# Kernel tuning notes

Hardware: AMD Instinct MI355X
Metric: run time of the kernel (lower is better)

## Reference

```python
import jax, jax.numpy as jnp
import numpy as np

D_CONV = 4
D_STATE = 32
DT_RANK = 16


def setup_inputs() -> dict:
    key = jax.random.key(0)
    ks = jax.random.split(key, 12)
    B, D, L, DI = 4, 256, 1024, 256
    s = 0.02
    return {
        "x": jax.random.normal(ks[0], (B, D, L), jnp.float32),
        "Win": jax.random.normal(ks[1], (4, D, 2 * DI), jnp.float32) * s,
        "Wconv": jax.random.normal(ks[2], (4, DI, D_CONV), jnp.float32) * 0.2,
        "bconv": jnp.zeros((4, DI), jnp.float32),
        "Wxp": jax.random.normal(ks[3], (4, DI, DT_RANK + 2 * D_STATE), jnp.float32) * s,
        "Wdt": jax.random.normal(ks[4], (4, DT_RANK, DI), jnp.float32) * s,
        "bdt": jnp.full((4, DI), -2.0, jnp.float32),
        "Alog": jnp.tile(jnp.log(jnp.arange(1, D_STATE + 1, dtype=jnp.float32))[None, None, :], (4, DI, 1)),
        "Dskip": jnp.ones((4, DI), jnp.float32),
        "Wout": jax.random.normal(ks[5], (4, DI, D), jnp.float32) * s,
        "Wg": jax.random.normal(ks[6], (2, L, L), jnp.float32) * 0.01,
        "bg": jnp.zeros((2, L), jnp.float32),
        "alpha": jnp.ones((2,), jnp.float32),
        "gamma": jnp.ones((2, L), jnp.float32),
        "beta": jnp.zeros((2, L), jnp.float32),
    }


def _selective_scan(u, dt, Bm, Cm, A):
    # u, dt: [B,L,di]; Bm, Cm: [B,L,N]; A: [di,N]
    dBu = dt * u
    def step(h, inp):
        dt_t, dbu_t, B_t, C_t = inp  # [B,di],[B,di],[B,N],[B,N]
        h = jnp.exp(dt_t[:, :, None] * A) * h + dbu_t[:, :, None] * B_t[:, None, :]
        y = jnp.einsum('bdn,bn->bd', h, C_t)
        return h, y
    xs = (jnp.moveaxis(dt, 1, 0), jnp.moveaxis(dBu, 1, 0),
          jnp.moveaxis(Bm, 1, 0), jnp.moveaxis(Cm, 1, 0))
    h0 = jnp.zeros((u.shape[0], A.shape[0], A.shape[1]), u.dtype)
    _, ys = jax.lax.scan(step, h0, xs)  # ys: [L,B,di]
    return jnp.moveaxis(ys, 0, 1)


def _mamba_layer(x_bdl, Win, Wconv, bconv, Wxp, Wdt, bdt, Alog, Dskip, Wout):
    x = jnp.swapaxes(x_bdl, 1, 2)  # [B,L,D]
    L = x.shape[1]
    u, z = jnp.split(x @ Win, 2, axis=-1)  # each [B,L,di]
    up = jnp.pad(u, ((0, 0), (D_CONV - 1, 0), (0, 0)))
    u = sum(up[:, k:k + L, :] * Wconv[:, k] for k in range(D_CONV)) + bconv
    u = jax.nn.silu(u)
    proj = u @ Wxp
    dtp = proj[..., :DT_RANK]
    Bm = proj[..., DT_RANK:DT_RANK + D_STATE]
    Cm = proj[..., DT_RANK + D_STATE:]
    dt = jax.nn.softplus(dtp @ Wdt + bdt)
    y = _selective_scan(u, dt, Bm, Cm, -jnp.exp(Alog)) + u * Dskip
    y = y * jax.nn.silu(z)
    return jnp.swapaxes(y @ Wout, 1, 2)  # [B,d_out,L]


def _forward(x, Win, Wconv, bconv, Wxp, Wdt, bdt, Alog, Dskip, Wout, Wg, bg, alpha, gamma, beta):
    def branch(inp, i0, i1, j):
        h = _mamba_layer(inp, Win[i0], Wconv[i0], bconv[i0], Wxp[i0], Wdt[i0], bdt[i0], Alog[i0], Dskip[i0], Wout[i0])
        h = _mamba_layer(h, Win[i1], Wconv[i1], bconv[i1], Wxp[i1], Wdt[i1], bdt[i1], Alog[i1], Dskip[i1], Wout[i1])
        return gamma[j] * jnp.tanh(alpha[j] * h) + beta[j]  # DyTanh over last dim
    def gate(j):
        return jax.nn.sigmoid(jnp.einsum('bdl,ml->bdm', x, Wg[j]) + bg[j])
    m = branch(x, 0, 1, 0) * gate(0)
    rx = jnp.flip(x, axis=-1)
    rm = branch(rx, 2, 3, 1) * gate(1)
    return m + jnp.flip(rm, axis=-1)


def reference(x, Win, Wconv, bconv, Wxp, Wdt, bdt, Alog, Dskip, Wout, Wg, bg, alpha, gamma, beta):
    return _forward(x, Win, Wconv, bconv, Wxp, Wdt, bdt, Alog, Dskip, Wout, Wg, bg, alpha, gamma, beta)
```

## Files before the change

### kernel.cpp

```cpp
#include <hip/hip_runtime.h>


#define LSEQ 1024
#define SCAN_CL 16
#define SCAN_NC 64

#if __has_builtin(__builtin_amdgcn_exp2f)
#define EXP2(x) __builtin_amdgcn_exp2f(x)
#else
#define EXP2(x) exp2f(x)
#endif

typedef short bf16x8 __attribute__((ext_vector_type(8)));
typedef float f32x4 __attribute__((ext_vector_type(4)));

__device__ __forceinline__ float sigmoidf_(float x) { return 1.f / (1.f + __expf(-x)); }
__device__ __forceinline__ float siluf_(float x)    { return x / (1.f + __expf(-x)); }
__device__ __forceinline__ float softplusf_(float x){ return x > 20.f ? x : log1pf(__expf(x)); }

__device__ __forceinline__ unsigned short bf16rne_(float v) {
  unsigned u = __float_as_uint(v);
  return (unsigned short)((u + 0x7FFFu + ((u >> 16) & 1u)) >> 16);
}
__device__ __forceinline__ float bfto_(unsigned short h) {
  return __uint_as_float(((unsigned)h) << 16);
}
__device__ __forceinline__ void split3_(float v, unsigned short& h,
                                        unsigned short& m, unsigned short& l) {
  h = bf16rne_(v); float r = v - bfto_(h);
  m = bf16rne_(r); float r2 = r - bfto_(m);
  l = bf16rne_(r2);
}

__device__ __forceinline__ long swzi(long idx, long row) {
  return idx ^ (((row >> 1) & 3) << 3);
}

__device__ void tconv3_body(const float* __restrict__ in,
                            unsigned short* __restrict__ oh,
                            unsigned short* __restrict__ om,
                            unsigned short* __restrict__ ol,
                            int K, int N, int bx, int by, int z) {
  __shared__ float T[32][33];
  int n0 = bx * 32, k0 = by * 32;
  int tx = threadIdx.x & 31, ty = threadIdx.x >> 5;
  const float* src = in + (long)z * K * N;
#pragma unroll
  for (int m = 0; m < 4; ++m)
    T[ty + 8 * m][tx] = src[(long)(k0 + ty + 8 * m) * N + n0 + tx];
  __syncthreads();
  long obase = (long)z * N * K;
#pragma unroll
  for (int m = 0; m < 4; ++m) {
    float v = T[tx][ty + 8 * m];
    int n = n0 + ty + 8 * m;
    long o = swzi(obase + (long)n * K + k0 + tx, n);
    split3_(v, oh[o], om[o], ol[o]);
  }
}

__device__ void split3v_body(const float4* __restrict__ in,
                             unsigned short* __restrict__ oh,
                             unsigned short* __restrict__ om,
                             unsigned short* __restrict__ ol, int i) {
  float4 v = in[i];
  long b = 4L * i;
  long sb = swzi(b, b >> 10);
  ushort4 H, M, L;
  split3_(v.x, H.x, M.x, L.x); split3_(v.y, H.y, M.y, L.y);
  split3_(v.z, H.z, M.z, L.z); split3_(v.w, H.w, M.w, L.w);
  *(ushort4*)(oh + sb) = H; *(ushort4*)(om + sb) = M; *(ushort4*)(ol + sb) = L;
}

__global__ __launch_bounds__(256)
void preprocess_kernel(const float* __restrict__ x, const float* __restrict__ Wg,
                       const float* __restrict__ Win, const float* __restrict__ Wout,
                       const float* __restrict__ Alog,
                       unsigned short* __restrict__ Xh, unsigned short* __restrict__ Xm,
                       unsigned short* __restrict__ Xl,
                       unsigned short* __restrict__ XGh, unsigned short* __restrict__ XGm,
                       unsigned short* __restrict__ XGl,
                       unsigned short* __restrict__ Wgh, unsigned short* __restrict__ Wgm,
                       unsigned short* __restrict__ Wgl,
                       unsigned short* __restrict__ WinTh, unsigned short* __restrict__ WinTm,
                       unsigned short* __restrict__ WinTl,
                       unsigned short* __restrict__ WoutTh, unsigned short* __restrict__ WoutTm,
                       unsigned short* __restrict__ WoutTl,
                       float* __restrict__ Aneg) {
  const int bid = blockIdx.x;
  if (bid < 8192) {
    long idx = (long)bid * 256 + threadIdx.x;
    int d = (int)(idx & 255);
    long t = idx >> 8;
    int l = (int)(t & 1023);
    int t2 = (int)(t >> 10);
    int b = t2 & 3;
    int j = t2 >> 2;
    int lsrc = j ? (1023 - l) : l;
    float v = x[((long)(b * 256 + d)) * LSEQ + lsrc];
    long o = swzi(idx, t);
    split3_(v, Xh[o], Xm[o], Xl[o]);
  } else if (bid < 9216) {
    int i = (bid - 8192) * 256 + threadIdx.x;
    split3v_body((const float4*)x, XGh, XGm, XGl, i);
  } else if (bid < 11264) {
    int i = (bid - 9216) * 256 + threadIdx.x;
    split3v_body((const float4*)Wg, Wgh, Wgm, Wgl, i);
  } else if (bid < 11776) {
    int t = bid - 11264;
    tconv3_body(Win, WinTh, WinTm, WinTl, 256, 512, t & 15, (t >> 4) & 7, t >> 7);
  } else if (bid < 12032) {
    int t = bid - 11776;
    tconv3_body(Wout, WoutTh, WoutTm, WoutTl, 256, 256, t & 7, (t >> 3) & 7, t >> 6);
  } else {
    int idx = (bid - 12032) * 256 + threadIdx.x;
    Aneg[idx] = -__expf(Alog[idx]) * 1.4426950408889634f;
  }
}

__device__ __forceinline__ void gload16(const unsigned short* g, unsigned short* l) {
  __builtin_amdgcn_global_load_lds(
      (const __attribute__((address_space(1))) unsigned int*)g,
      (__attribute__((address_space(3))) unsigned int*)l, 16, 0, 0);
}

template <int KSPLIT>
__global__ __launch_bounds__(256)
void gemm_mfma(const unsigned short* __restrict__ Ah_g,
               const unsigned short* __restrict__ Am_g,
               const unsigned short* __restrict__ Al_g, long aZ, int lda,
               const unsigned short* __restrict__ Bh_g,
               const unsigned short* __restrict__ Bm_g,
               const unsigned short* __restrict__ Bl_g, long bZ, int ldb,
               float* __restrict__ C, long cZ, int N, int KH) {
  __shared__ unsigned short S[2][6][128 * 32];
  const int bz = blockIdx.z;
  const int z  = (KSPLIT == 2) ? (bz >> 1) : bz;
  const int kh = (KSPLIT == 2) ? (bz & 1) : 0;
  const int m0 = blockIdx.y * 128, n0 = blockIdx.x * 128;
  const int tid = threadIdx.x;

  const long khoff = (long)kh * KH;
  const long a0 = (long)z * aZ + (long)(m0 + (tid >> 2)) * lda + khoff + (tid & 3) * 8;
  const long a1 = a0 + 64L * lda;
  const long b0 = (long)z * bZ + (long)(n0 + (tid >> 2)) * ldb + khoff + (tid & 3) * 8;
  const long b1 = b0 + 64L * ldb;
  const int l0 = tid * 8, l1 = tid * 8 + 2048;

  const int lane = tid & 63, w = tid >> 6;
  const int wr = w >> 1, wc = w & 1;
  const int fr = lane & 15, g = lane >> 4;

  f32x4 acc[4][4];
#pragma unroll
  for (int i = 0; i < 4; ++i)
#pragma unroll
    for (int j = 0; j < 4; ++j)
#pragma unroll
      for (int q = 0; q < 4; ++q) acc[i][j][q] = 0.f;

#define ISSUE_TILE(B, KOFF)                                 \
  do {                                                      \
    gload16(Ah_g + a0 + (KOFF), &S[B][0][l0]);              \
    gload16(Ah_g + a1 + (KOFF), &S[B][0][l1]);              \
    gload16(Am_g + a0 + (KOFF), &S[B][1][l0]);              \
    gload16(Am_g + a1 + (KOFF), &S[B][1][l1]);              \
    gload16(Al_g + a0 + (KOFF), &S[B][2][l0]);              \
    gload16(Al_g + a1 + (KOFF), &S[B][2][l1]);              \
    gload16(Bh_g + b0 + (KOFF), &S[B][3][l0]);              \
    gload16(Bh_g + b1 + (KOFF), &S[B][3][l1]);              \
    gload16(Bm_g + b0 + (KOFF), &S[B][4][l0]);              \
    gload16(Bm_g + b1 + (KOFF), &S[B][4][l1]);              \
    gload16(Bl_g + b0 + (KOFF), &S[B][5][l0]);              \
    gload16(Bl_g + b1 + (KOFF), &S[B][5][l1]);              \
  } while (0)

  ISSUE_TILE(0, 0);
  int cur = 0;

  for (int k0 = 0; k0 < KH; k0 += 32) {
    asm volatile("s_waitcnt lgkmcnt(0)" ::: "memory");
    __builtin_amdgcn_s_barrier();
    if (k0 + 32 < KH) {
      ISSUE_TILE(cur ^ 1, k0 + 32);
      asm volatile("s_waitcnt vmcnt(12)" ::: "memory");
    } else {
      asm volatile("s_waitcnt vmcnt(0)" ::: "memory");
    }
    __builtin_amdgcn_s_barrier();
    __builtin_amdgcn_sched_barrier(0);

    bf16x8 fb[3][4];
#pragma unroll
    for (int nf = 0; nf < 4; ++nf) {
      int rb = wc * 64 + nf * 16 + fr;
      int ob = rb * 32 + ((g ^ ((rb >> 1) & 3)) << 3);
      fb[0][nf] = *(const bf16x8*)&S[cur][3][ob];
      fb[1][nf] = *(const bf16x8*)&S[cur][4][ob];
      fb[2][nf] = *(const bf16x8*)&S[cur][5][ob];
    }
#pragma unroll
    for (int mf = 0; mf < 4; ++mf) {
      int ra = wr * 64 + mf * 16 + fr;
      int oa = ra * 32 + ((g ^ ((ra >> 1) & 3)) << 3);
      bf16x8 fah = *(const bf16x8*)&S[cur][0][oa];
      bf16x8 fam = *(const bf16x8*)&S[cur][1][oa];
      bf16x8 fal = *(const bf16x8*)&S[cur][2][oa];
#pragma unroll
      for (int nf = 0; nf < 4; ++nf) {
        acc[mf][nf] = __builtin_amdgcn_mfma_f32_16x16x32_bf16(fah, fb[0][nf], acc[mf][nf], 0, 0, 0);
        acc[mf][nf] = __builtin_amdgcn_mfma_f32_16x16x32_bf16(fah, fb[1][nf], acc[mf][nf], 0, 0, 0);
        acc[mf][nf] = __builtin_amdgcn_mfma_f32_16x16x32_bf16(fam, fb[0][nf], acc[mf][nf], 0, 0, 0);
        acc[mf][nf] = __builtin_amdgcn_mfma_f32_16x16x32_bf16(fam, fb[1][nf], acc[mf][nf], 0, 0, 0);
        acc[mf][nf] = __builtin_amdgcn_mfma_f32_16x16x32_bf16(fah, fb[2][nf], acc[mf][nf], 0, 0, 0);
        acc[mf][nf] = __builtin_amdgcn_mfma_f32_16x16x32_bf16(fal, fb[0][nf], acc[mf][nf], 0, 0, 0);
      }
    }
    cur ^= 1;
  }
#undef ISSUE_TILE

  float* Cz = C + (long)bz * cZ;
#pragma unroll
  for (int mf = 0; mf < 4; ++mf)
#pragma unroll
    for (int nf = 0; nf < 4; ++nf) {
      int col = n0 + wc * 64 + nf * 16 + fr;
      int row0 = m0 + wr * 64 + mf * 16 + g * 4;
#pragma unroll
      for (int q = 0; q < 4; ++q)
        Cz[(long)(row0 + q) * N + col] = acc[mf][nf][q];
    }
}

template <int OP>
__global__ __launch_bounds__(256)
void combine2_kernel(const float* __restrict__ P, long pz,
                     const float* __restrict__ bias, int nmask,
                     float* __restrict__ outF,
                     unsigned short* __restrict__ oh,
                     unsigned short* __restrict__ om,
                     unsigned short* __restrict__ ol, long oz) {
  int z = blockIdx.y;
  long i = (long)blockIdx.x * 256 + threadIdx.x;
  float v = P[(long)(2 * z) * pz + i] + P[(long)(2 * z + 1) * pz + i];
  if (OP == 1) {
    outF[(long)z * oz + i] = sigmoidf_(v + bias[z * (nmask + 1) + (int)(i & nmask)]);
  } else {
    long o = (long)z * oz + swzi(i, i >> 8);
    split3_(v, oh[o], om[o], ol[o]);
  }
}

__global__ __launch_bounds__(256)
void gemm23_kernel(const float* __restrict__ UZ, const float* __restrict__ Wconv,
                   const float* __restrict__ bconv,
                   const float* __restrict__ Wxp,
                   const float* __restrict__ Wdt, const float* __restrict__ bdt,
                   float* __restrict__ UC, float* __restrict__ PROJ,
                   float* __restrict__ DTo, int stage) {
  __shared__ float UZt[19][256];
  __shared__ float ucs[16][260];
  __shared__ float Ws[16][80];
  __shared__ float PR[16][17];
  __shared__ float WD[16][256];
  const int z = blockIdx.y;
  const int lidx = stage + 2 * z;
  const int m0 = blockIdx.x * 16;
  const int l0 = m0 & 1023;
  const float* W = Wxp + (long)lidx * 256 * 80;
  const int tid = threadIdx.x;
  const int tx = tid & 15, ty = tid >> 4;

#pragma unroll
  for (int t = 0; t < 16; ++t) {
    int e = t * 256 + tid;
    WD[e >> 8][e & 255] = Wdt[(long)lidx * 4096 + e];
  }

  {
    const long base = ((long)z * 4096 + m0 - 3) * 512 + tid;
#pragma unroll
    for (int r = 0; r < 19; ++r)
      UZt[r][tid] = (l0 == 0 && r < 3) ? 0.f : UZ[base + (long)r * 512];
  }
  __syncthreads();

  {
    const float* wcp = Wconv + (long)(lidx * 256 + tid) * 4;
    float w0 = wcp[0], w1 = wcp[1], w2 = wcp[2], w3 = wcp[3];
    float bcv = bconv[lidx * 256 + tid];
#pragma unroll
    for (int it = 0; it < 16; ++it) {
      float acc = bcv;
      acc = fmaf(UZt[it + 0][tid], w0, acc);
      acc = fmaf(UZt[it + 1][tid], w1, acc);
      acc = fmaf(UZt[it + 2][tid], w2, acc);
      acc = fmaf(UZt[it + 3][tid], w3, acc);
      float ucv = acc * sigmoidf_(acc);
      UC[((long)z * 4096 + m0 + it) * 256 + tid] = ucv;
      ucs[it][tid] = ucv;
    }
  }
  __syncthreads();

  float acc[5];
#pragma unroll
  for (int j = 0; j < 5; ++j) acc[j] = 0.f;

  for (int k0 = 0; k0 < 256; k0 += 16) {
    {
      int k = tid >> 4, cg2 = (tid & 15) * 5;
#pragma unroll
      for (int i2 = 0; i2 < 5; ++i2)
        Ws[k][cg2 + i2] = W[(long)(k0 + k) * 80 + cg2 + i2];
    }
    __syncthreads();
#pragma unroll
    for (int kk = 0; kk < 16; ++kk) {
      float a = ucs[ty][k0 + kk];
#pragma unroll
      for (int j = 0; j < 5; ++j)
        acc[j] = fmaf(a, Ws[kk][tx * 5 + j], acc[j]);
    }
    __syncthreads();
  }

#pragma unroll
  for (int j = 0; j < 5; ++j) {
    int c = tx * 5 + j;
    float v = acc[j];
    PROJ[((long)z * 4096 + m0 + ty) * 80 + c] = v;
    if (c < 16) PR[ty][c] = v;
  }
  __syncthreads();

  for (int it = 0; it < 16; ++it) {
    float ssum = 0.f;
#pragma unroll
    for (int k = 0; k < 16; ++k) ssum = fmaf(PR[it][k], WD[k][tid], ssum);
    DTo[((long)z * 4096 + m0 + it) * 256 + tid] =
        softplusf_(ssum + bdt[lidx * 256 + tid]);
  }
}

template <int PASS>
__global__ __launch_bounds__(256)
void scan_chunk_kernel(const float* __restrict__ dt,
                       const float* __restrict__ uc,
                       const float* __restrict__ UZ,
                       const float* __restrict__ proj,
                       const float* __restrict__ Aneg,
                       const float* __restrict__ Dskip,
                       float* __restrict__ HST,
                       float* __restrict__ DTS,
                       unsigned short* __restrict__ YGh,
                       unsigned short* __restrict__ YGm,
                       unsigned short* __restrict__ YGl, int stage) {
  __shared__ __align__(16) float BC[SCAN_CL][64];
  const int blk = blockIdx.x;
  const int c128 = blk & 1;
  const int chunk = (blk >> 1) & (SCAN_NC - 1);
  const int jb = blk >> 7;
  const int tid = threadIdx.x;
  const int di = c128 * 128 + (tid >> 1);
  const int nh = tid & 1;
  const int j = jb >> 2;
  const int lidx = stage + 2 * j;
  const long r0 = (long)jb * 1024 + (long)chunk * SCAN_CL;

  for (int e = tid; e < SCAN_CL * 64; e += 256) {
    int l = e >> 6, col = e & 63;
    BC[l][col] = proj[(r0 + l) * 80 + 16 + col];
  }

  float A[16];
  {
    const float4* ap = (const float4*)(Aneg + ((long)(lidx * 256 + di)) * 32 + nh * 16);
#pragma unroll
    for (int q = 0; q < 4; ++q) {
      float4 v = ap[q];
      A[4 * q] = v.x; A[4 * q + 1] = v.y; A[4 * q + 2] = v.z; A[4 * q + 3] = v.w;
    }
  }

  const long sbase = (((long)jb * SCAN_NC + chunk) * 256 + di) * 32 + nh * 16;
  float h[16];
  if (PASS == 0) {
#pragma unroll
    for (int n = 0; n < 16; ++n) h[n] = 0.f;
  } else {
    const float4* hp = (const float4*)(HST + sbase);
#pragma unroll
    for (int q = 0; q < 4; ++q) {
      float4 v = hp[q];
      h[4 * q] = v.x; h[4 * q + 1] = v.y; h[4 * q + 2] = v.z; h[4 * q + 3] = v.w;
    }
  }

  float Dsk = 0.f, dtsum = 0.f;
  if (PASS == 1) Dsk = Dskip[lidx * 256 + di];

  const float* dtp = dt + r0 * 256 + di;
  const float* up  = uc + r0 * 256 + di;
  const float* zp  = UZ + r0 * 512 + 256 + di;

  __syncthreads();

  float Db[2][8], Ub[2][8], Zb[2][8];
#pragma unroll
  for (int i = 0; i < 8; ++i) {
    Db[0][i] = dtp[(long)i * 256];
    Ub[0][i] = up[(long)i * 256];
    if (PASS == 1) Zb[0][i] = zp[(long)i * 512];
  }

#pragma unroll
  for (int bt = 0; bt < SCAN_CL / 8; ++bt) {
    const int cur = bt & 1, nxt = cur ^ 1;
    if (bt < SCAN_CL / 8 - 1) {
#pragma unroll
      for (int i = 0; i < 8; ++i) {
        long l = (long)(bt + 1) * 8 + i;
        Db[nxt][i] = dtp[l * 256];
        Ub[nxt][i] = up[l * 256];
        if (PASS == 1) Zb[nxt][i] = zp[l * 512];
      }
    }
#pragma unroll
    for (int i = 0; i < 8; ++i) {
      const int l = bt * 8 + i;
      float dtv = Db[cur][i];
      float uv  = Ub[cur][i];
      float du  = dtv * uv;
      if (PASS == 0) dtsum += dtv;
      float yacc[4] = {0.f, 0.f, 0.f, 0.f};
      const float4* bc4 = (const float4*)&BC[l][nh * 16];
      const float4* cc4 = (const float4*)&BC[l][32 + nh * 16];
#pragma unroll
      for (int q = 0; q < 4; ++q) {
        float4 bv = bc4[q];
        float4 cv = cc4[q];
        const float* bp = &bv.x;
        const float* cp = &cv.x;
#pragma unroll
        for (int k = 0; k < 4; ++k) {
          int n = 4 * q + k;
          float a = EXP2(dtv * A[n]);
          h[n] = fmaf(a, h[n], du * bp[k]);
          yacc[k] = fmaf(h[n], cp[k], yacc[k]);
        }
      }
      if (PASS == 1) {
        float p = (yacc[0] + yacc[1]) + (yacc[2] + yacc[3]);
        p += __shfl_xor(p, 1);
        if (nh == 0) {
          float zv = Zb[cur][i];
          float val = (p + uv * Dsk) * siluf_(zv);
          long o = swzi((r0 + l) * 256 + di, r0 + l);
          split3_(val, YGh[o], YGm[o], YGl[o]);
        }
      }
    }
  }

  if (PASS == 0) {
    float4* hp = (float4*)(HST + sbase);
#pragma unroll
    for (int q = 0; q < 4; ++q)
      hp[q] = make_float4(h[4 * q], h[4 * q + 1], h[4 * q + 2], h[4 * q + 3]);
    if (nh == 0)
      DTS[((long)jb * SCAN_NC + chunk) * 256 + di] = dtsum;
  }
}

__global__ __launch_bounds__(256)
void scan_combine_kernel(float* __restrict__ HST, const float* __restrict__ DTS,
                         const float* __restrict__ Aneg, int stage) {
  int t = blockIdx.x * 256 + threadIdx.x;
  int n = t & 31;
  int di = (t >> 5) & 255;
  int jb = t >> 13;
  int lidx = stage + 2 * (jb >> 2);
  float A = Aneg[((long)(lidx * 256 + di)) * 32 + n];
  float hs = 0.f;
  for (int cb = 0; cb < SCAN_NC; cb += 8) {
    float s[8], P[8], hv[8];
#pragma unroll
    for (int i = 0; i < 8; ++i) {
      long base = ((long)jb * SCAN_NC + cb + i) * 256 + di;
      s[i] = HST[base * 32 + n];
      P[i] = DTS[base];
    }
#pragma unroll
    for (int i = 0; i < 8; ++i) P[i] = EXP2(A * P[i]);
#pragma unroll
    for (int i = 0; i < 8; ++i) {
      hv[i] = hs;
      hs = fmaf(P[i], hs, s[i]);
    }
#pragma unroll
    for (int i = 0; i < 8; ++i) {
      long base = ((long)jb * SCAN_NC + cb + i) * 256 + di;
      HST[base * 32 + n] = hv[i];
    }
  }
}

__global__ __launch_bounds__(256) void combine_kernel(const float* __restrict__ PG,
                                                      long pz,
                                                      const float* __restrict__ gate,
                                                      const float* __restrict__ alpha,
                                                      const float* __restrict__ gamma,
                                                      const float* __restrict__ beta,
                                                      float* __restrict__ out) {
  long idx = (long)blockIdx.x * 256 + threadIdx.x;
  int l = (int)(idx & 1023);
  long t = idx >> 10;
  int d = (int)(t & 255);
  int b = (int)(t >> 8);
  int lr = 1023 - l;
  long b0 = ((long)(b * 1024 + l)) * 256 + d;
  long b1 = ((long)(b * 1024 + lr)) * 256 + d;
  float h0 = PG[b0] + PG[pz + b0];
  float h1 = PG[2 * pz + b1] + PG[3 * pz + b1];
  float g0 = gate[((long)(b * 256 + d)) * 1024 + l];
  float g1 = gate[(long)1024 * 1024 + ((long)(b * 256 + d)) * 1024 + lr];
  float m0 = (gamma[l] * tanhf(alpha[0] * h0) + beta[l]) * g0;
  float m1 = (gamma[1024 + lr] * tanhf(alpha[1] * h1) + beta[1024 + lr]) * g1;
  out[idx] = m0 + m1;
}

extern "C" void kernel_launch(void* const* d_in, const int* in_sizes, int n_in,
                              void* d_out, int out_size, void* d_ws, size_t ws_size,
                              hipStream_t stream) {
  const float* x     = (const float*)d_in[0];
  const float* Win   = (const float*)d_in[1];
  const float* Wconv = (const float*)d_in[2];
  const float* bconv = (const float*)d_in[3];
  const float* Wxp   = (const float*)d_in[4];
  const float* Wdt   = (const float*)d_in[5];
  const float* bdt   = (const float*)d_in[6];
  const float* Alog  = (const float*)d_in[7];
  const float* Dskip = (const float*)d_in[8];
  const float* Wout  = (const float*)d_in[9];
  const float* Wg    = (const float*)d_in[10];
  const float* bg    = (const float*)d_in[11];
  const float* alpha = (const float*)d_in[12];
  const float* gamma = (const float*)d_in[13];
  const float* beta  = (const float*)d_in[14];
  float* out = (float*)d_out;

  float* ws   = (float*)d_ws;
  float* UZ   = ws;
  float* UC   = UZ + 4194304;
  float* PROJ = UC + 2097152;
  float* DT   = PROJ + 655360;
  float* GATE = DT + 2097152;
  float* ANEG = GATE + 2097152;
  float* HST  = ANEG + 32768;
  float* DTS  = HST + 4194304;
  float* PG   = DTS + 131072;
  unsigned short* Xpl  = (unsigned short*)(PG + 4194304);
  unsigned short* YGpl = Xpl + 3 * 2097152;
  unsigned short* XGpl = YGpl + 3 * 2097152;
  unsigned short* Wgpl = XGpl + 3 * 1048576;
  unsigned short* WinT = Wgpl + 3 * 2097152;
  unsigned short* WoutT = WinT + 3 * 524288;
  unsigned short* Xh = Xpl, *Xm = Xpl + 2097152, *Xl = Xpl + 2 * 2097152;
  unsigned short* YGh = YGpl, *YGm = YGpl + 2097152, *YGl = YGpl + 2 * 2097152;
  unsigned short* XGh = XGpl, *XGm = XGpl + 1048576, *XGl = XGpl + 2 * 1048576;
  unsigned short* Wgh = Wgpl, *Wgm = Wgpl + 2097152, *Wgl = Wgpl + 2 * 2097152;
  unsigned short* WinTh = WinT, *WinTm = WinT + 524288, *WinTl = WinT + 2 * 524288;
  unsigned short* WoutTh = WoutT, *WoutTm = WoutT + 262144, *WoutTl = WoutT + 2 * 262144;

  preprocess_kernel<<<dim3(12160), dim3(256), 0, stream>>>(
      x, Wg, Win, Wout, Alog, Xh, Xm, Xl, XGh, XGm, XGl,
      Wgh, Wgm, Wgl, WinTh, WinTm, WinTl, WoutTh, WoutTm, WoutTl, ANEG);

  gemm_mfma<2><<<dim3(8, 8, 4), dim3(256), 0, stream>>>(
      XGh, XGm, XGl, 0L, 1024,
      Wgh, Wgm, Wgl, (long)1024 * 1024, 1024,
      PG, (long)1024 * 1024, 1024, 512);
  combine2_kernel<1><<<dim3(4096, 2), dim3(256), 0, stream>>>(
      PG, (long)1024 * 1024, bg, 1023, GATE, nullptr, nullptr, nullptr,
      (long)1024 * 1024);

  for (int s = 0; s < 2; ++s) {
    gemm_mfma<1><<<dim3(4, 32, 2), dim3(256), 0, stream>>>(
        Xh, Xm, Xl, (long)4096 * 256, 256,
        WinTh + (long)s * 131072, WinTm + (long)s * 131072, WinTl + (long)s * 131072,
        (long)262144, 256,
        UZ, (long)4096 * 512, 512, 256);

    gemm23_kernel<<<dim3(256, 2), dim3(256), 0, stream>>>(
        UZ, Wconv, bconv, Wxp, Wdt, bdt, UC, PROJ, DT, s);

    scan_chunk_kernel<0><<<dim3(2 * 8 * SCAN_NC), dim3(256), 0, stream>>>(
        DT, UC, UZ, PROJ, ANEG, Dskip, HST, DTS, YGh, YGm, YGl, s);
    scan_combine_kernel<<<dim3(256), dim3(256), 0, stream>>>(HST, DTS, ANEG, s);
    scan_chunk_kernel<1><<<dim3(2 * 8 * SCAN_NC), dim3(256), 0, stream>>>(
        DT, UC, UZ, PROJ, ANEG, Dskip, HST, DTS, YGh, YGm, YGl, s);

    gemm_mfma<2><<<dim3(2, 32, 4), dim3(256), 0, stream>>>(
        YGh, YGm, YGl, (long)4096 * 256, 256,
        WoutTh + (long)s * 65536, WoutTm + (long)s * 65536, WoutTl + (long)s * 65536,
        (long)131072, 256,
        PG, (long)4096 * 256, 256, 128);
    if (s == 0) {
      combine2_kernel<2><<<dim3(4096, 2), dim3(256), 0, stream>>>(
          PG, (long)4096 * 256, nullptr, 0, nullptr, Xh, Xm, Xl, (long)4096 * 256);
    }
  }

  combine_kernel<<<dim3(4096), dim3(256), 0, stream>>>(
      PG, (long)4096 * 256, GATE, alpha, gamma, beta, out);
}
```

Measured before the change: 286.9 us.

## Fold gate sigmoid into final combine and split-K the input projection GEMM

```diff
diff --git a/kernel.cpp b/kernel.cpp
--- a/kernel.cpp
+++ b/kernel.cpp
@@ -4,6 +4,7 @@
 #define LSEQ 1024
 #define SCAN_CL 16
 #define SCAN_NC 64
+#define G1PLANE 2097152L
 
 #if __has_builtin(__builtin_amdgcn_exp2f)
 #define EXP2(x) __builtin_amdgcn_exp2f(x)
@@ -236,7 +237,6 @@
 template <int OP>
 __global__ __launch_bounds__(256)
 void combine2_kernel(const float* __restrict__ P, long pz,
-                     const float* __restrict__ bias, int nmask,
                      float* __restrict__ outF,
                      unsigned short* __restrict__ oh,
                      unsigned short* __restrict__ om,
@@ -244,8 +244,8 @@
   int z = blockIdx.y;
   long i = (long)blockIdx.x * 256 + threadIdx.x;
   float v = P[(long)(2 * z) * pz + i] + P[(long)(2 * z + 1) * pz + i];
-  if (OP == 1) {
-    outF[(long)z * oz + i] = sigmoidf_(v + bias[z * (nmask + 1) + (int)(i & nmask)]);
+  if (OP == 0) {
+    outF[(long)z * oz + i] = v;
   } else {
     long o = (long)z * oz + swzi(i, i >> 8);
     split3_(v, oh[o], om[o], ol[o]);
@@ -253,7 +253,7 @@
 }
 
 __global__ __launch_bounds__(256)
-void gemm23_kernel(const float* __restrict__ UZ, const float* __restrict__ Wconv,
+void gemm23_kernel(const float* __restrict__ PG1, const float* __restrict__ Wconv,
                    const float* __restrict__ bconv,
                    const float* __restrict__ Wxp,
                    const float* __restrict__ Wdt, const float* __restrict__ bdt,
@@ -279,10 +279,13 @@
   }
 
   {
-    const long base = ((long)z * 4096 + m0 - 3) * 512 + tid;
+    const long base = (long)(z * 2) * G1PLANE + ((long)(m0 - 3)) * 512 + tid;
 #pragma unroll
     for (int r = 0; r < 19; ++r)
-      UZt[r][tid] = (l0 == 0 && r < 3) ? 0.f : UZ[base + (long)r * 512];
+      UZt[r][tid] = (l0 == 0 && r < 3)
+                        ? 0.f
+                        : (PG1[base + (long)r * 512] +
+                           PG1[base + G1PLANE + (long)r * 512]);
   }
   __syncthreads();
 
@@ -348,7 +351,7 @@
 __global__ __launch_bounds__(256)
 void scan_chunk_kernel(const float* __restrict__ dt,
                        const float* __restrict__ uc,
-                       const float* __restrict__ UZ,
+                       const float* __restrict__ PG1,
                        const float* __restrict__ proj,
                        const float* __restrict__ Aneg,
                        const float* __restrict__ Dskip,
@@ -403,7 +406,8 @@
 
   const float* dtp = dt + r0 * 256 + di;
   const float* up  = uc + r0 * 256 + di;
-  const float* zp  = UZ + r0 * 512 + 256 + di;
+  const float* zp0 = PG1 + (long)(j * 2) * G1PLANE + (r0 & 4095) * 512 + 256 + di;
+  const float* zp1 = zp0 + G1PLANE;
 
   __syncthreads();
 
@@ -412,7 +416,7 @@
   for (int i = 0; i < 8; ++i) {
     Db[0][i] = dtp[(long)i * 256];
     Ub[0][i] = up[(long)i * 256];
-    if (PASS == 1) Zb[0][i] = zp[(long)i * 512];
+    if (PASS == 1) Zb[0][i] = zp0[(long)i * 512] + zp1[(long)i * 512];
   }
 
 #pragma unroll
@@ -424,7 +428,7 @@
         long l = (long)(bt + 1) * 8 + i;
         Db[nxt][i] = dtp[l * 256];
         Ub[nxt][i] = up[l * 256];
-        if (PASS == 1) Zb[nxt][i] = zp[l * 512];
+        if (PASS == 1) Zb[nxt][i] = zp0[l * 512] + zp1[l * 512];
       }
     }
 #pragma unroll
@@ -509,11 +513,13 @@
 
 __global__ __launch_bounds__(256) void combine_kernel(const float* __restrict__ PG,
                                                       long pz,
-                                                      const float* __restrict__ gate,
+                                                      const float* __restrict__ PGATE,
+                                                      const float* __restrict__ bg,
                                                       const float* __restrict__ alpha,
                                                       const float* __restrict__ gamma,
                                                       const float* __restrict__ beta,
                                                       float* __restrict__ out) {
+  const long GZ = 1024L * 1024;
   long idx = (long)blockIdx.x * 256 + threadIdx.x;
   int l = (int)(idx & 1023);
   long t = idx >> 10;
@@ -524,8 +530,10 @@
   long b1 = ((long)(b * 1024 + lr)) * 256 + d;
   float h0 = PG[b0] + PG[pz + b0];
   float h1 = PG[2 * pz + b1] + PG[3 * pz + b1];
-  float g0 = gate[((long)(b * 256 + d)) * 1024 + l];
-  float g1 = gate[(long)1024 * 1024 + ((long)(b * 256 + d)) * 1024 + lr];
+  long gi0 = ((long)(b * 256 + d)) * 1024 + l;
+  long gi1 = ((long)(b * 256 + d)) * 1024 + lr;
+  float g0 = sigmoidf_((PGATE[gi0] + PGATE[GZ + gi0]) + bg[l]);
+  float g1 = sigmoidf_((PGATE[2 * GZ + gi1] + PGATE[3 * GZ + gi1]) + bg[1024 + lr]);
   float m0 = (gamma[l] * tanhf(alpha[0] * h0) + beta[l]) * g0;
   float m1 = (gamma[1024 + lr] * tanhf(alpha[1] * h1) + beta[1024 + lr]) * g1;
   out[idx] = m0 + m1;
@@ -551,16 +559,16 @@
   const float* beta  = (const float*)d_in[14];
   float* out = (float*)d_out;
 
-  float* ws   = (float*)d_ws;
-  float* UZ   = ws;
-  float* UC   = UZ + 4194304;
-  float* PROJ = UC + 2097152;
-  float* DT   = PROJ + 655360;
-  float* GATE = DT + 2097152;
-  float* ANEG = GATE + 2097152;
-  float* HST  = ANEG + 32768;
-  float* DTS  = HST + 4194304;
-  float* PG   = DTS + 131072;
+  float* ws    = (float*)d_ws;
+  float* PG1   = ws;
+  float* UC    = PG1 + 8388608;
+  float* PROJ  = UC + 2097152;
+  float* DT    = PROJ + 655360;
+  float* PGATE = DT + 2097152;
+  float* ANEG  = PGATE + 4194304;
+  float* HST   = ANEG + 32768;
+  float* DTS   = HST + 4194304;
+  float* PG    = DTS + 131072;
   unsigned short* Xpl  = (unsigned short*)(PG + 4194304);
   unsigned short* YGpl = Xpl + 3 * 2097152;
   unsigned short* XGpl = YGpl + 3 * 2097152;
@@ -581,26 +589,23 @@
   gemm_mfma<2><<<dim3(8, 8, 4), dim3(256), 0, stream>>>(
       XGh, XGm, XGl, 0L, 1024,
       Wgh, Wgm, Wgl, (long)1024 * 1024, 1024,
-      PG, (long)1024 * 1024, 1024, 512);
-  combine2_kernel<1><<<dim3(4096, 2), dim3(256), 0, stream>>>(
-      PG, (long)1024 * 1024, bg, 1023, GATE, nullptr, nullptr, nullptr,
-      (long)1024 * 1024);
+      PGATE, (long)1024 * 1024, 1024, 512);
 
   for (int s = 0; s < 2; ++s) {
-    gemm_mfma<1><<<dim3(4, 32, 2), dim3(256), 0, stream>>>(
+    gemm_mfma<2><<<dim3(4, 32, 4), dim3(256), 0, stream>>>(
         Xh, Xm, Xl, (long)4096 * 256, 256,
         WinTh + (long)s * 131072, WinTm + (long)s * 131072, WinTl + (long)s * 131072,
         (long)262144, 256,
-        UZ, (long)4096 * 512, 512, 256);
+        PG1, G1PLANE, 512, 128);
 
     gemm23_kernel<<<dim3(256, 2), dim3(256), 0, stream>>>(
-        UZ, Wconv, bconv, Wxp, Wdt, bdt, UC, PROJ, DT, s);
+        PG1, Wconv, bconv, Wxp, Wdt, bdt, UC, PROJ, DT, s);
 
     scan_chunk_kernel<0><<<dim3(2 * 8 * SCAN_NC), dim3(256), 0, stream>>>(
-        DT, UC, UZ, PROJ, ANEG, Dskip, HST, DTS, YGh, YGm, YGl, s);
+        DT, UC, PG1, PROJ, ANEG, Dskip, HST, DTS, YGh, YGm, YGl, s);
     scan_combine_kernel<<<dim3(256), dim3(256), 0, stream>>>(HST, DTS, ANEG, s);
     scan_chunk_kernel<1><<<dim3(2 * 8 * SCAN_NC), dim3(256), 0, stream>>>(
-        DT, UC, UZ, PROJ, ANEG, Dskip, HST, DTS, YGh, YGm, YGl, s);
+        DT, UC, PG1, PROJ, ANEG, Dskip, HST, DTS, YGh, YGm, YGl, s);
 
     gemm_mfma<2><<<dim3(2, 32, 4), dim3(256), 0, stream>>>(
         YGh, YGm, YGl, (long)4096 * 256, 256,
@@ -609,10 +614,10 @@
         PG, (long)4096 * 256, 256, 128);
     if (s == 0) {
       combine2_kernel<2><<<dim3(4096, 2), dim3(256), 0, stream>>>(
-          PG, (long)4096 * 256, nullptr, 0, nullptr, Xh, Xm, Xl, (long)4096 * 256);
+          PG, (long)4096 * 256, nullptr, Xh, Xm, Xl, (long)4096 * 256);
     }
   }
 
   combine_kernel<<<dim3(4096), dim3(256), 0, stream>>>(
-      PG, (long)4096 * 256, GATE, alpha, gamma, beta, out);
-}
+      PG, (long)4096 * 256, PGATE, bg, alpha, gamma, beta, out);
+}
```

New measurement: 294.0 us. 1.02x slower.
